# Kernel optimization log

Measured on AMD Instinct MI355X. Metric: run time of the kernel, lower is better.

Reference implementation:

```python
import jax, jax.numpy as jnp
import numpy as np

NEG_INF = -1e30

def _mask_logits(t, m):
    m = m.astype(jnp.float32)
    return t * m + (1.0 - m) * NEG_INF

def setup_inputs() -> dict:
    key = jax.random.key(0)
    ks = jax.random.split(key, 8)
    B, Lc, Lq, D = 16, 2048, 512, 512
    C = jax.random.normal(ks[0], (B, Lc, D), dtype=jnp.float32)
    Q = jax.random.normal(ks[1], (B, Lq, D), dtype=jnp.float32)
    Cmask = jax.random.randint(ks[2], (B, Lc), 0, 2, dtype=jnp.int32)
    Qmask = jax.random.randint(ks[3], (B, Lq), 0, 2, dtype=jnp.int32)
    W1 = jax.random.normal(ks[4], (D, D), dtype=jnp.float32) * (1.0 / np.sqrt(D))
    b1 = jnp.zeros((D,), dtype=jnp.float32)
    Wf = jax.random.normal(ks[5], (4 * D, 4 * D), dtype=jnp.float32) * (1.0 / np.sqrt(4 * D))
    bf = jnp.zeros((4 * D,), dtype=jnp.float32)
    Wg = jax.random.normal(ks[6], (4 * D, 4 * D), dtype=jnp.float32) * (1.0 / np.sqrt(4 * D))
    bg = jnp.zeros((4 * D,), dtype=jnp.float32)
    return {"C": C, "Q": Q, "Cmask": Cmask, "Qmask": Qmask,
            "W1": W1, "b1": b1, "Wf": Wf, "bf": bf, "Wg": Wg, "bg": bg}

def reference(C, Q, Cmask, Qmask, W1, b1, Wf, bf, Wg, bg):
    C_ = jax.nn.leaky_relu(C @ W1.T + b1)          # [B, Lc, D]
    Q_ = jax.nn.leaky_relu(Q @ W1.T + b1)          # [B, Lq, D]
    S = jnp.einsum('bcd,bqd->bcq', C_, Q_)         # [B, Lc, Lq]
    Cm = Cmask[:, :, None]                          # [B, Lc, 1]
    Qm = Qmask[:, None, :]                          # [B, 1, Lq]
    S = _mask_logits(_mask_logits(S, Cm), Qm)
    S_ = jax.nn.softmax(S, axis=2)
    attn_C = jnp.einsum('bcq,bqd->bcd', S_, Q)     # [B, Lc, D]
    cat = jnp.concatenate([C, attn_C, attn_C - C, attn_C * C], axis=2)  # [B, Lc, 4D]
    fuse = jnp.tanh(cat @ Wf.T + bf)
    gate = jax.nn.sigmoid(cat @ Wg.T + bg)
    out = gate * fuse + (1.0 - gate) * cat
    out = _mask_logits(out, Cm)
    return out
```

## Files before the change

### kernel.cpp

```cpp
#include <hip/hip_runtime.h>
#include <hip/hip_bf16.h>
#include <math.h>

using bf16 = __hip_bfloat16;
typedef __attribute__((ext_vector_type(8))) short s16x8;
typedef __attribute__((ext_vector_type(4))) float f32x4;
typedef __attribute__((ext_vector_type(8))) int i32x8;
typedef __attribute__((ext_vector_type(4))) int i32x4;

#define NEG_INF_F (-1e30f)

static constexpr int BATCH = 16;
static constexpr int LC = 2048;
static constexpr int LQ = 512;
static constexpr int DIM = 512;
static constexpr int FEAT = 2048;
static constexpr int MC = BATCH * LC;
static constexpr int MQ = BATCH * LQ;

__device__ __forceinline__ float bfs2f(short s) {
    union { float f; unsigned u; } x;
    x.u = ((unsigned)(unsigned short)s) << 16;
    return x.f;
}
__device__ __forceinline__ short f2bfs(float f) {
    bf16 h = __float2bfloat16(f);
    short s; __builtin_memcpy(&s, &h, 2);
    return s;
}
__device__ __forceinline__ float fp8_to_f(unsigned b) {
    const unsigned s = b >> 7, e = (b >> 3) & 15, m = b & 7;
    const int ee = e ? (int)e : 1;
    const int mm = e ? (int)(8 + m) : (int)m;
    union { unsigned u; float f; } sc; sc.u = (unsigned)(ee + 117) << 23;
    const float v = (float)mm * sc.f;
    return s ? -v : v;
}
__device__ __forceinline__ uint2 pk8fp8(float a0, float a1, float a2, float a3,
                                        float a4, float a5, float a6, float a7) {
    uint2 r;
    int w0 = __builtin_amdgcn_cvt_pk_fp8_f32(a0, a1, 0, false);
    w0 = __builtin_amdgcn_cvt_pk_fp8_f32(a2, a3, w0, true);
    int w1 = __builtin_amdgcn_cvt_pk_fp8_f32(a4, a5, 0, false);
    w1 = __builtin_amdgcn_cvt_pk_fp8_f32(a6, a7, w1, true);
    r.x = (unsigned)w0; r.y = (unsigned)w1;
    return r;
}

#define GLL(gp, lp) __builtin_amdgcn_global_load_lds( \
    (const __attribute__((address_space(1))) void*)(gp), \
    (__attribute__((address_space(3))) void*)(lp), 16, 0, 0)

__global__ __launch_bounds__(256) void cvt_f32_bf16(const float* __restrict__ in,
                                                    bf16* __restrict__ out, int n) {
    int i = (blockIdx.x * 256 + threadIdx.x) * 4;
    if (i + 3 < n) {
        float4 v = *(const float4*)(in + i);
        ushort4 o;
        o.x = (unsigned short)f2bfs(v.x);
        o.y = (unsigned short)f2bfs(v.y);
        o.z = (unsigned short)f2bfs(v.z);
        o.w = (unsigned short)f2bfs(v.w);
        *(ushort4*)(out + i) = o;
    } else {
        for (int k = i; k < n; k++) out[k] = __float2bfloat16(in[k]);
    }
}

__global__ __launch_bounds__(256) void cvt_f32_fp8_w(const float* __restrict__ in,
                                                     unsigned char* __restrict__ out, int n) {
    int i = (blockIdx.x * 256 + threadIdx.x) * 4;
    if (i >= n) return;
    float4 v = *(const float4*)(in + i);
    int w0 = __builtin_amdgcn_cvt_pk_fp8_f32(v.x * 32.f, v.y * 32.f, 0, false);
    w0 = __builtin_amdgcn_cvt_pk_fp8_f32(v.z * 32.f, v.w * 32.f, w0, true);
    *(int*)(out + i) = w0;
}

__global__ __launch_bounds__(256) void transpose_q(const float* __restrict__ Q,
                                                   bf16* __restrict__ Qt) {
    __shared__ float t[32][33];
    const int b = blockIdx.z;
    const int q0 = blockIdx.x * 32, d0 = blockIdx.y * 32;
    const int tx = threadIdx.x, ty = threadIdx.y;
    const float* Qb = Q + (long)b * LQ * DIM;
    bf16* Qtb = Qt + (long)b * DIM * LQ;
#pragma unroll
    for (int i = 0; i < 32; i += 8)
        t[ty + i][tx] = Qb[(long)(q0 + ty + i) * DIM + d0 + tx];
    __syncthreads();
#pragma unroll
    for (int i = 0; i < 32; i += 8)
        Qtb[(long)(d0 + ty + i) * LQ + q0 + tx] = __float2bfloat16(t[tx][ty + i]);
}

__global__ __launch_bounds__(256) void mask_count(const int* __restrict__ cm,
                                                  int* __restrict__ cnt) {
    const int b = blockIdx.x;
    const int* p = cm + b * LC;
    int s = 0;
    for (int i = threadIdx.x; i < LC; i += 256) s += p[i] ? 1 : 0;
#pragma unroll
    for (int o = 32; o > 0; o >>= 1) s += __shfl_down(s, o, 64);
    __shared__ int red[4];
    if ((threadIdx.x & 63) == 0) red[threadIdx.x >> 6] = s;
    __syncthreads();
    if (threadIdx.x == 0) cnt[b] = red[0] + red[1] + red[2] + red[3];
}
__global__ void mask_scan(const int* __restrict__ cnt, int* __restrict__ off) {
    if (threadIdx.x == 0) {
        int a = 0;
        for (int b = 0; b < BATCH; b++) { off[b] = a; a += cnt[b]; }
        off[BATCH] = a;
    }
}
__global__ __launch_bounds__(256) void mask_compact(const int* __restrict__ cm,
                                                    const int* __restrict__ off,
                                                    int* __restrict__ idx) {
    const int b = blockIdx.x;
    const int tid = threadIdx.x;
    const int lane = tid & 63, wv = tid >> 6;
    const int* p = cm + b * LC + tid * 8;
    int f[8], ls = 0;
#pragma unroll
    for (int i = 0; i < 8; i++) { f[i] = p[i] ? 1 : 0; ls += f[i]; }
    int inc = ls;
#pragma unroll
    for (int o = 1; o < 64; o <<= 1) {
        int y = __shfl_up(inc, o, 64);
        if (lane >= o) inc += y;
    }
    __shared__ int wsum[4];
    if (lane == 63) wsum[wv] = inc;
    __syncthreads();
    int base = off[b];
    for (int w = 0; w < wv; w++) base += wsum[w];
    int ex = base + inc - ls;
    const int orig = b * LC + tid * 8;
    for (int i = 0; i < 8; i++)
        if (f[i]) idx[ex++] = orig + i;
}

__global__ __launch_bounds__(256) void fill_masked(float* __restrict__ out,
                                                   const int* __restrict__ cm) {
    const float4 v = make_float4(NEG_INF_F, NEG_INF_F, NEG_INF_F, NEG_INF_F);
    const long total = (long)MC * (FEAT / 4);
    const long stride = (long)gridDim.x * 256;
    for (long p = (long)blockIdx.x * 256 + threadIdx.x; p < total; p += stride) {
        const int row = (int)(p >> 9);
        if (cm[row] == 0) ((float4*)out)[p] = v;
    }
}

enum { MODE_PLAIN = 0, MODE_BIAS_LRELU = 1 };

template <int MODE>
__global__ __launch_bounds__(256)
void gemm_bt(const bf16* __restrict__ A, const bf16* __restrict__ B,
             void* __restrict__ Out,
             const float* __restrict__ bias,
             int N, int K,
             long strideA, long strideB, long strideO) {
    constexpr int BM = 128, BN = 128, BK = 32;
    __shared__ __align__(16) bf16 As[BM * BK];
    __shared__ __align__(16) bf16 Bs[BN * BK];

    const int z = blockIdx.z;
    const bf16* Ab = A + (long)z * strideA;
    const bf16* Bb = B + (long)z * strideB;

    const int tid = threadIdx.x;
    const int wave = tid >> 6, lane = tid & 63;
    const int wm = (wave >> 1) * 64, wn = (wave & 1) * 64;
    const int lrow = lane & 15, lq = lane >> 4;

    const int bm0 = blockIdx.y * BM;
    const int bn0 = blockIdx.x * BN;

    const int srow = tid >> 2;
    const int scol = (tid & 3) * 8;

    const bf16* ag = Ab + (long)(bm0 + srow) * K + scol;
    const bf16* bg = Bb + (long)(bn0 + srow) * K + scol;
    bf16* asl = &As[srow * BK + scol];
    bf16* bsl = &Bs[srow * BK + scol];
    const long skip64 = (long)64 * K;

    f32x4 acc[4][4];
#pragma unroll
    for (int i = 0; i < 4; i++)
#pragma unroll
        for (int j = 0; j < 4; j++) acc[i][j] = (f32x4){0.f, 0.f, 0.f, 0.f};

    for (int k0 = 0; k0 < K; k0 += BK) {
        GLL(ag, asl);
        GLL(ag + skip64, asl + 64 * BK);
        GLL(bg, bsl);
        GLL(bg + skip64, bsl + 64 * BK);
        ag += BK; bg += BK;
        __syncthreads();

        s16x8 af[4], bfv[4];
#pragma unroll
        for (int f = 0; f < 4; f++)
            af[f] = *(const s16x8*)&As[(wm + f * 16 + lrow) * BK + lq * 8];
#pragma unroll
        for (int f = 0; f < 4; f++)
            bfv[f] = *(const s16x8*)&Bs[(wn + f * 16 + lrow) * BK + lq * 8];

#pragma unroll
        for (int i = 0; i < 4; i++)
#pragma unroll
            for (int j = 0; j < 4; j++)
                acc[i][j] = __builtin_amdgcn_mfma_f32_16x16x32_bf16(af[i], bfv[j], acc[i][j], 0, 0, 0);
        __syncthreads();
    }

#pragma unroll
    for (int i = 0; i < 4; i++) {
#pragma unroll
        for (int j = 0; j < 4; j++) {
            const int n = bn0 + wn + j * 16 + lrow;
            const float bn_bias = (MODE == MODE_PLAIN) ? 0.f : bias[n];
#pragma unroll
            for (int r = 0; r < 4; r++) {
                const int m = bm0 + wm + i * 16 + lq * 4 + r;
                const long off = (long)z * strideO + (long)m * N + n;
                float v = acc[i][j][r];
                if (MODE == MODE_PLAIN) {
                    ((bf16*)Out)[off] = __float2bfloat16(v);
                } else {
                    v += bn_bias;
                    v = v > 0.f ? v : 0.01f * v;
                    ((bf16*)Out)[off] = __float2bfloat16(v);
                }
            }
        }
    }
}

__global__ __launch_bounds__(256, 2)
void gemm_dual_fp8(const unsigned char* __restrict__ A8,
                   const unsigned char* __restrict__ Bf8,
                   const unsigned char* __restrict__ Bg8,
                   float* __restrict__ Out,
                   const float* __restrict__ biasf, const float* __restrict__ biasg,
                   const int* __restrict__ idx,
                   const int* __restrict__ offs) {
    constexpr int BM = 128, BN = 128;
    constexpr int N = FEAT, K = FEAT;
    __shared__ __align__(16) char As[BM * 128];
    __shared__ __align__(16) char Bfs[BN * 128];
    __shared__ __align__(16) char Bgs[BN * 128];

    const int Mp = offs[BATCH];
    const int bm0 = blockIdx.y * BM;
    if (bm0 >= Mp) return;
    const int bn0 = blockIdx.x * BN;

    const int tid = threadIdx.x;
    const int wave = tid >> 6, lane = tid & 63;
    const int wm = (wave >> 1) * 64, wn = (wave & 1) * 64;
    const int lrow = lane & 15, lq = lane >> 4;

    const int p = tid & 7, r0 = tid >> 3;
    const int xo = (p ^ (r0 & 7)) * 16;
    const unsigned char* agp = A8 + (long)(bm0 + r0) * K + xo;
    const unsigned char* bfgp = Bf8 + (long)(bn0 + r0) * K + xo;
    const unsigned char* bggp = Bg8 + (long)(bn0 + r0) * K + xo;
    char* asl = As + tid * 16;
    char* bfl = Bfs + tid * 16;
    char* bgl = Bgs + tid * 16;
    const long rowskip = (long)32 * K;

    int offA0[4], offA1[4], offB0[4], offB1[4];
#pragma unroll
    for (int f = 0; f < 4; f++) {
        const int ra = wm + f * 16 + lrow;
        offA0[f] = ra * 128 + (((lq * 2 + 0) ^ (ra & 7)) * 16);
        offA1[f] = ra * 128 + (((lq * 2 + 1) ^ (ra & 7)) * 16);
        const int rb = wn + f * 16 + lrow;
        offB0[f] = rb * 128 + (((lq * 2 + 0) ^ (rb & 7)) * 16);
        offB1[f] = rb * 128 + (((lq * 2 + 1) ^ (rb & 7)) * 16);
    }

    f32x4 accf[4][4], accg[4][4];
#pragma unroll
    for (int i = 0; i < 4; i++)
#pragma unroll
        for (int j = 0; j < 4; j++) {
            accf[i][j] = (f32x4){0.f, 0.f, 0.f, 0.f};
            accg[i][j] = (f32x4){0.f, 0.f, 0.f, 0.f};
        }

    for (int k0 = 0; k0 < K; k0 += 128) {
#pragma unroll
        for (int r = 0; r < 4; r++) {
            GLL(agp + (long)r * rowskip, asl + r * 4096);
            GLL(bfgp + (long)r * rowskip, bfl + r * 4096);
            GLL(bggp + (long)r * rowskip, bgl + r * 4096);
        }
        agp += 128; bfgp += 128; bggp += 128;
        __syncthreads();

        i32x8 af[4];
#pragma unroll
        for (int f = 0; f < 4; f++) {
            const i32x4 lo = *(const i32x4*)(As + offA0[f]);
            const i32x4 hi = *(const i32x4*)(As + offA1[f]);
            af[f][0] = lo[0]; af[f][1] = lo[1]; af[f][2] = lo[2]; af[f][3] = lo[3];
            af[f][4] = hi[0]; af[f][5] = hi[1]; af[f][6] = hi[2]; af[f][7] = hi[3];
        }
#pragma unroll
        for (int j = 0; j < 4; j++) {
            i32x8 bfj, bgj;
            {
                const i32x4 lo = *(const i32x4*)(Bfs + offB0[j]);
                const i32x4 hi = *(const i32x4*)(Bfs + offB1[j]);
                bfj[0] = lo[0]; bfj[1] = lo[1]; bfj[2] = lo[2]; bfj[3] = lo[3];
                bfj[4] = hi[0]; bfj[5] = hi[1]; bfj[6] = hi[2]; bfj[7] = hi[3];
            }
            {
                const i32x4 lo = *(const i32x4*)(Bgs + offB0[j]);
                const i32x4 hi = *(const i32x4*)(Bgs + offB1[j]);
                bgj[0] = lo[0]; bgj[1] = lo[1]; bgj[2] = lo[2]; bgj[3] = lo[3];
                bgj[4] = hi[0]; bgj[5] = hi[1]; bgj[6] = hi[2]; bgj[7] = hi[3];
            }
#pragma unroll
            for (int i = 0; i < 4; i++)
                accf[i][j] = __builtin_amdgcn_mfma_scale_f32_16x16x128_f8f6f4(
                    af[i], bfj, accf[i][j], 0, 0, 0, 127, 0, 122);
#pragma unroll
            for (int i = 0; i < 4; i++)
                accg[i][j] = __builtin_amdgcn_mfma_scale_f32_16x16x128_f8f6f4(
                    af[i], bgj, accg[i][j], 0, 0, 0, 127, 0, 122);
        }
        __syncthreads();
    }

#pragma unroll
    for (int j = 0; j < 4; j++) {
        const int n = bn0 + wn + j * 16 + lrow;
        const float bfb = biasf[n];
        const float bgb = biasg[n];
#pragma unroll
        for (int i = 0; i < 4; i++) {
#pragma unroll
            for (int r = 0; r < 4; r++) {
                const int m = bm0 + wm + i * 16 + lq * 4 + r;
                if (m < Mp) {
                    const float vf = accf[i][j][r] + bfb;
                    const float vg = accg[i][j][r] + bgb;
                    const float e = __expf(2.0f * fabsf(vf));
                    const float th = copysignf(1.0f - 2.0f / (e + 1.0f), vf);
                    const float g = 1.0f / (1.0f + __expf(-vg));
                    const float c = fp8_to_f(A8[(long)m * N + n]);
                    Out[(long)idx[m] * N + n] = g * th + (1.0f - g) * c;
                }
            }
        }
    }
}

__global__ __launch_bounds__(256) void softmax_rows(bf16* __restrict__ S,
                                                    const int* __restrict__ Cmask,
                                                    const int* __restrict__ Qmask) {
    const int row = blockIdx.x * 4 + (threadIdx.x >> 6);
    const int lane = threadIdx.x & 63;
    const int b = row >> 11;
    bf16* srow = S + (long)row * LQ;
    short* sp = (short*)srow + lane * 8;

    if (Cmask[row] == 0) {
        const short u = f2bfs(1.0f / 512.0f);
        s16x8 uv;
#pragma unroll
        for (int i = 0; i < 8; i++) uv[i] = u;
        *(s16x8*)sp = uv;
        return;
    }

    const int* qm = Qmask + b * LQ + lane * 8;
    const int4 m0 = *(const int4*)(qm);
    const int4 m1 = *(const int4*)(qm + 4);
    const int msk[8] = {m0.x, m0.y, m0.z, m0.w, m1.x, m1.y, m1.z, m1.w};
    const s16x8 sv = *(const s16x8*)sp;

    float v[8];
    float mx = -3e38f;
#pragma unroll
    for (int i = 0; i < 8; i++) {
        v[i] = msk[i] ? bfs2f(sv[i]) : -3e38f;
        mx = fmaxf(mx, v[i]);
    }
#pragma unroll
    for (int o = 32; o > 0; o >>= 1) mx = fmaxf(mx, __shfl_xor(mx, o, 64));

    float e[8];
    float s = 0.f;
#pragma unroll
    for (int i = 0; i < 8; i++) {
        e[i] = msk[i] ? __expf(v[i] - mx) : 0.f;
        s += e[i];
    }
#pragma unroll
    for (int o = 32; o > 0; o >>= 1) s += __shfl_xor(s, o, 64);

    s16x8 ov;
    if (!(s > 0.f)) {
        const short u = f2bfs(1.0f / 512.0f);
#pragma unroll
        for (int i = 0; i < 8; i++) ov[i] = u;
    } else {
        const float inv = 1.0f / s;
#pragma unroll
        for (int i = 0; i < 8; i++) ov[i] = f2bfs(e[i] * inv);
    }
    *(s16x8*)sp = ov;
}

__global__ __launch_bounds__(256) void build_cat(const bf16* __restrict__ Cb,
                                                 const bf16* __restrict__ attn,
                                                 unsigned char* __restrict__ cat8,
                                                 const int* __restrict__ idx,
                                                 const int* __restrict__ offs) {
    const long t = (long)blockIdx.x * 256 + threadIdx.x;
    const int j = (int)(t >> 6);
    if (j >= offs[BATCH]) return;
    const int m = idx[j];
    const int c = (int)(t & 63) << 3;
    const s16x8 cv = *(const s16x8*)((const short*)Cb + (long)m * DIM + c);
    const s16x8 av = *(const s16x8*)((const short*)attn + (long)m * DIM + c);
    float cf[8], af_[8];
#pragma unroll
    for (int i = 0; i < 8; i++) { cf[i] = bfs2f(cv[i]); af_[i] = bfs2f(av[i]); }
    unsigned char* rowp = cat8 + (long)j * FEAT + c;
    *(uint2*)(rowp) = pk8fp8(cf[0], cf[1], cf[2], cf[3], cf[4], cf[5], cf[6], cf[7]);
    *(uint2*)(rowp + 512) = pk8fp8(af_[0], af_[1], af_[2], af_[3], af_[4], af_[5], af_[6], af_[7]);
    *(uint2*)(rowp + 1024) = pk8fp8(af_[0] - cf[0], af_[1] - cf[1], af_[2] - cf[2], af_[3] - cf[3],
                                    af_[4] - cf[4], af_[5] - cf[5], af_[6] - cf[6], af_[7] - cf[7]);
    *(uint2*)(rowp + 1536) = pk8fp8(af_[0] * cf[0], af_[1] * cf[1], af_[2] * cf[2], af_[3] * cf[3],
                                    af_[4] * cf[4], af_[5] * cf[5], af_[6] * cf[6], af_[7] * cf[7]);
}

extern "C" void kernel_launch(void* const* d_in, const int* in_sizes, int n_in,
                              void* d_out, int out_size, void* d_ws, size_t ws_size,
                              hipStream_t stream) {
    (void)in_sizes; (void)n_in; (void)out_size; (void)ws_size;
    const float* C = (const float*)d_in[0];
    const float* Q = (const float*)d_in[1];
    const int* Cmask = (const int*)d_in[2];
    const int* Qmask = (const int*)d_in[3];
    const float* W1 = (const float*)d_in[4];
    const float* b1 = (const float*)d_in[5];
    const float* Wf = (const float*)d_in[6];
    const float* bfp = (const float*)d_in[7];
    const float* Wg = (const float*)d_in[8];
    const float* bgp = (const float*)d_in[9];
    float* out = (float*)d_out;

    char* ws = (char*)d_ws;
    unsigned char* cat8 = (unsigned char*)(ws + 0);
    bf16* W1b  = (bf16*)(ws + 0);
    bf16* Qb   = (bf16*)(ws + 524288);
    bf16* Qt   = (bf16*)(ws + 8912896);
    bf16* C_   = (bf16*)(ws + 17301504);
    bf16* Q_   = (bf16*)(ws + 50855936);
    bf16* S    = (bf16*)(ws + 59244544);
    int*  idx  = (int*)(ws + 92798976);
    int*  cnts = (int*)(ws + 92930048);
    int*  offs = (int*)(ws + 92930112);
    bf16* Cb   = (bf16*)(ws + 134217728);
    bf16* attn = (bf16*)(ws + 167772160);
    unsigned char* Wf8 = (unsigned char*)(ws + 201326592);
    unsigned char* Wg8 = (unsigned char*)(ws + 205520896);

    mask_count<<<BATCH, 256, 0, stream>>>(Cmask, cnts);
    mask_scan<<<1, 64, 0, stream>>>(cnts, offs);
    mask_compact<<<BATCH, 256, 0, stream>>>(Cmask, offs, idx);

    cvt_f32_bf16<<<256, 256, 0, stream>>>(W1, W1b, DIM * DIM);
    cvt_f32_fp8_w<<<4096, 256, 0, stream>>>(Wf, Wf8, FEAT * FEAT);
    cvt_f32_fp8_w<<<4096, 256, 0, stream>>>(Wg, Wg8, FEAT * FEAT);
    cvt_f32_bf16<<<16384, 256, 0, stream>>>(C, Cb, MC * DIM);
    cvt_f32_bf16<<<4096, 256, 0, stream>>>(Q, Qb, MQ * DIM);
    transpose_q<<<dim3(16, 16, 16), dim3(32, 8), 0, stream>>>(Q, Qt);

    gemm_bt<MODE_BIAS_LRELU><<<dim3(4, 256, 1), 256, 0, stream>>>(
        Cb, W1b, C_, b1, DIM, DIM, 0, 0, 0);
    gemm_bt<MODE_BIAS_LRELU><<<dim3(4, 64, 1), 256, 0, stream>>>(
        Qb, W1b, Q_, b1, DIM, DIM, 0, 0, 0);

    gemm_bt<MODE_PLAIN><<<dim3(4, 16, 16), 256, 0, stream>>>(
        C_, Q_, S, nullptr, LQ, DIM,
        (long)LC * DIM, (long)LQ * DIM, (long)LC * LQ);

    softmax_rows<<<MC / 4, 256, 0, stream>>>(S, Cmask, Qmask);

    gemm_bt<MODE_PLAIN><<<dim3(4, 16, 16), 256, 0, stream>>>(
        S, Qt, attn, nullptr, DIM, LQ,
        (long)LC * LQ, (long)DIM * LQ, (long)LC * DIM);

    build_cat<<<8192, 256, 0, stream>>>(Cb, attn, cat8, idx, offs);

    fill_masked<<<4096, 256, 0, stream>>>(out, Cmask);

    gemm_dual_fp8<<<dim3(16, 256, 1), 256, 0, stream>>>(
        cat8, Wf8, Wg8, out, bfp, bgp, idx, offs);
}
```

Baseline: 733.2 us.

## Compact unmasked context rows through projection, similarity, softmax and attention stages

Gathers and converts only the unmasked context rows into a compacted bf16 buffer. The C projection GEMM, the per-batch similarity GEMM, the softmax and the attention GEMM then run on compacted rows, using offsets and early exits on blocks with no valid rows. This removes roughly half of the upstream GEMM and softmax work that was previously spent on rows whose outputs are overwritten by the mask. In exchange the GEMM tiles may read past the valid rows into neighbouring data (writes are guarded), and the kernels take extra indirection through idx and offs.

```diff
diff --git a/kernel.cpp b/kernel.cpp
--- a/kernel.cpp
+++ b/kernel.cpp
@@ -141,6 +141,22 @@
         if (f[i]) idx[ex++] = orig + i;
 }
 
+__global__ __launch_bounds__(128) void gather_cvt_c(const float* __restrict__ C,
+                                                    const int* __restrict__ idx,
+                                                    const int* __restrict__ offs,
+                                                    bf16* __restrict__ Cbc) {
+    const int j = blockIdx.x;
+    if (j >= offs[BATCH]) return;
+    const int m = idx[j];
+    const float4 v = ((const float4*)(C + (long)m * DIM))[threadIdx.x];
+    ushort4 o;
+    o.x = (unsigned short)f2bfs(v.x);
+    o.y = (unsigned short)f2bfs(v.y);
+    o.z = (unsigned short)f2bfs(v.z);
+    o.w = (unsigned short)f2bfs(v.w);
+    ((ushort4*)(Cbc + (long)j * DIM))[threadIdx.x] = o;
+}
+
 __global__ __launch_bounds__(256) void fill_masked(float* __restrict__ out,
                                                    const int* __restrict__ cm) {
     const float4 v = make_float4(NEG_INF_F, NEG_INF_F, NEG_INF_F, NEG_INF_F);
@@ -160,13 +176,29 @@
              void* __restrict__ Out,
              const float* __restrict__ bias,
              int N, int K,
-             long strideA, long strideB, long strideO) {
+             long strideA, long strideB, long strideO,
+             const int* __restrict__ offs, int cmode) {
     constexpr int BM = 128, BN = 128, BK = 32;
     __shared__ __align__(16) bf16 As[BM * BK];
     __shared__ __align__(16) bf16 Bs[BN * BK];
 
     const int z = blockIdx.z;
-    const bf16* Ab = A + (long)z * strideA;
+    const int bm0 = blockIdx.y * BM;
+    long aBase, oBase;
+    int rows_left;
+    if (cmode == 0) {
+        aBase = (long)z * strideA; oBase = (long)z * strideO; rows_left = 1 << 30;
+    } else if (cmode == 1) {
+        aBase = 0; oBase = 0;
+        rows_left = offs[BATCH] - bm0;
+        if (rows_left <= 0) return;
+    } else {
+        const int o0 = offs[z], o1 = offs[z + 1];
+        aBase = (long)o0 * K; oBase = (long)o0 * N;
+        rows_left = (o1 - o0) - bm0;
+        if (rows_left <= 0) return;
+    }
+    const bf16* Ab = A + aBase;
     const bf16* Bb = B + (long)z * strideB;
 
     const int tid = threadIdx.x;
@@ -174,7 +206,6 @@
     const int wm = (wave >> 1) * 64, wn = (wave & 1) * 64;
     const int lrow = lane & 15, lq = lane >> 4;
 
-    const int bm0 = blockIdx.y * BM;
     const int bn0 = blockIdx.x * BN;
 
     const int srow = tid >> 2;
@@ -224,15 +255,17 @@
             const float bn_bias = (MODE == MODE_PLAIN) ? 0.f : bias[n];
 #pragma unroll
             for (int r = 0; r < 4; r++) {
-                const int m = bm0 + wm + i * 16 + lq * 4 + r;
-                const long off = (long)z * strideO + (long)m * N + n;
-                float v = acc[i][j][r];
-                if (MODE == MODE_PLAIN) {
-                    ((bf16*)Out)[off] = __float2bfloat16(v);
-                } else {
-                    v += bn_bias;
-                    v = v > 0.f ? v : 0.01f * v;
-                    ((bf16*)Out)[off] = __float2bfloat16(v);
+                const int mloc = wm + i * 16 + lq * 4 + r;
+                if (mloc < rows_left) {
+                    const long off = oBase + (long)(bm0 + mloc) * N + n;
+                    float v = acc[i][j][r];
+                    if (MODE == MODE_PLAIN) {
+                        ((bf16*)Out)[off] = __float2bfloat16(v);
+                    } else {
+                        v += bn_bias;
+                        v = v > 0.f ? v : 0.01f * v;
+                        ((bf16*)Out)[off] = __float2bfloat16(v);
+                    }
                 }
             }
         }
@@ -363,22 +396,15 @@
 }
 
 __global__ __launch_bounds__(256) void softmax_rows(bf16* __restrict__ S,
-                                                    const int* __restrict__ Cmask,
+                                                    const int* __restrict__ idx,
+                                                    const int* __restrict__ offs,
                                                     const int* __restrict__ Qmask) {
     const int row = blockIdx.x * 4 + (threadIdx.x >> 6);
+    if (row >= offs[BATCH]) return;
     const int lane = threadIdx.x & 63;
-    const int b = row >> 11;
+    const int b = idx[row] >> 11;
     bf16* srow = S + (long)row * LQ;
     short* sp = (short*)srow + lane * 8;
-
-    if (Cmask[row] == 0) {
-        const short u = f2bfs(1.0f / 512.0f);
-        s16x8 uv;
-#pragma unroll
-        for (int i = 0; i < 8; i++) uv[i] = u;
-        *(s16x8*)sp = uv;
-        return;
-    }
 
     const int* qm = Qmask + b * LQ + lane * 8;
     const int4 m0 = *(const int4*)(qm);
@@ -419,18 +445,16 @@
     *(s16x8*)sp = ov;
 }
 
-__global__ __launch_bounds__(256) void build_cat(const bf16* __restrict__ Cb,
-                                                 const bf16* __restrict__ attn,
+__global__ __launch_bounds__(256) void build_cat(const bf16* __restrict__ Cbc,
+                                                 const bf16* __restrict__ attnc,
                                                  unsigned char* __restrict__ cat8,
-                                                 const int* __restrict__ idx,
                                                  const int* __restrict__ offs) {
     const long t = (long)blockIdx.x * 256 + threadIdx.x;
     const int j = (int)(t >> 6);
     if (j >= offs[BATCH]) return;
-    const int m = idx[j];
     const int c = (int)(t & 63) << 3;
-    const s16x8 cv = *(const s16x8*)((const short*)Cb + (long)m * DIM + c);
-    const s16x8 av = *(const s16x8*)((const short*)attn + (long)m * DIM + c);
+    const s16x8 cv = *(const s16x8*)((const short*)Cbc + (long)j * DIM + c);
+    const s16x8 av = *(const s16x8*)((const short*)attnc + (long)j * DIM + c);
     float cf[8], af_[8];
 #pragma unroll
     for (int i = 0; i < 8; i++) { cf[i] = bfs2f(cv[i]); af_[i] = bfs2f(av[i]); }
@@ -464,14 +488,14 @@
     bf16* W1b  = (bf16*)(ws + 0);
     bf16* Qb   = (bf16*)(ws + 524288);
     bf16* Qt   = (bf16*)(ws + 8912896);
-    bf16* C_   = (bf16*)(ws + 17301504);
+    bf16* C_c  = (bf16*)(ws + 17301504);
     bf16* Q_   = (bf16*)(ws + 50855936);
-    bf16* S    = (bf16*)(ws + 59244544);
+    bf16* Sc   = (bf16*)(ws + 59244544);
     int*  idx  = (int*)(ws + 92798976);
     int*  cnts = (int*)(ws + 92930048);
     int*  offs = (int*)(ws + 92930112);
-    bf16* Cb   = (bf16*)(ws + 134217728);
-    bf16* attn = (bf16*)(ws + 167772160);
+    bf16* Cbc  = (bf16*)(ws + 134217728);
+    bf16* attnc= (bf16*)(ws + 167772160);
     unsigned char* Wf8 = (unsigned char*)(ws + 201326592);
     unsigned char* Wg8 = (unsigned char*)(ws + 205520896);
 
@@ -482,26 +506,26 @@
     cvt_f32_bf16<<<256, 256, 0, stream>>>(W1, W1b, DIM * DIM);
     cvt_f32_fp8_w<<<4096, 256, 0, stream>>>(Wf, Wf8, FEAT * FEAT);
     cvt_f32_fp8_w<<<4096, 256, 0, stream>>>(Wg, Wg8, FEAT * FEAT);
-    cvt_f32_bf16<<<16384, 256, 0, stream>>>(C, Cb, MC * DIM);
+    gather_cvt_c<<<MC, 128, 0, stream>>>(C, idx, offs, Cbc);
     cvt_f32_bf16<<<4096, 256, 0, stream>>>(Q, Qb, MQ * DIM);
     transpose_q<<<dim3(16, 16, 16), dim3(32, 8), 0, stream>>>(Q, Qt);
 
     gemm_bt<MODE_BIAS_LRELU><<<dim3(4, 256, 1), 256, 0, stream>>>(
-        Cb, W1b, C_, b1, DIM, DIM, 0, 0, 0);
+        Cbc, W1b, C_c, b1, DIM, DIM, 0, 0, 0, offs, 1);
     gemm_bt<MODE_BIAS_LRELU><<<dim3(4, 64, 1), 256, 0, stream>>>(
-        Qb, W1b, Q_, b1, DIM, DIM, 0, 0, 0);
+        Qb, W1b, Q_, b1, DIM, DIM, 0, 0, 0, nullptr, 0);
 
     gemm_bt<MODE_PLAIN><<<dim3(4, 16, 16), 256, 0, stream>>>(
-        C_, Q_, S, nullptr, LQ, DIM,
-        (long)LC * DIM, (long)LQ * DIM, (long)LC * LQ);
-
-    softmax_rows<<<MC / 4, 256, 0, stream>>>(S, Cmask, Qmask);
+        C_c, Q_, Sc, nullptr, LQ, DIM,
+        0, (long)LQ * DIM, 0, offs, 2);
+
+    softmax_rows<<<MC / 4, 256, 0, stream>>>(Sc, idx, offs, Qmask);
 
     gemm_bt<MODE_PLAIN><<<dim3(4, 16, 16), 256, 0, stream>>>(
-        S, Qt, attn, nullptr, DIM, LQ,
-        (long)LC * LQ, (long)DIM * LQ, (long)LC * DIM);
-
-    build_cat<<<8192, 256, 0, stream>>>(Cb, attn, cat8, idx, offs);
+        Sc, Qt, attnc, nullptr, DIM, LQ,
+        0, (long)DIM * LQ, 0, offs, 2);
+
+    build_cat<<<8192, 256, 0, stream>>>(Cbc, attnc, cat8, offs);
 
     fill_masked<<<4096, 256, 0, stream>>>(out, Cmask);
 
```

Measured after the change: 716.8 us. -2.2%, faster.
